# Performance work log

Hardware: AMD Instinct MI355X
Metric: run time of the kernel (lower is better)

## Reference

```python
import jax, jax.numpy as jnp
import numpy as np

N_NODES = 20000
N_EDGES = 320000
N_GRAPHS = 64
NEG_SLOPE = 0.2


def gat_conv(h, src, dst, a_src, a_dst, n_nodes):
    # h: [N, H, C] transformed node features; src/dst: [E] with self loops
    al_s = jnp.sum(h * a_src, axis=-1)  # [N, H]
    al_d = jnp.sum(h * a_dst, axis=-1)  # [N, H]
    e = jax.nn.leaky_relu(al_s[src] + al_d[dst], NEG_SLOPE)  # [E, H]
    m = jax.ops.segment_max(e, dst, num_segments=n_nodes)  # [N, H]
    ex = jnp.exp(e - m[dst])
    denom = jax.ops.segment_sum(ex, dst, num_segments=n_nodes)
    alpha = ex / denom[dst]  # [E, H] segment softmax over incoming edges
    # weighted scatter-aggregate of source features
    out = jax.ops.segment_sum(alpha[:, :, None] * h[src], dst, num_segments=n_nodes)
    return out  # [N, H, C]


def setup_inputs() -> dict:
    key = jax.random.key(0)
    ks = jax.random.split(key, 12)
    x = jax.random.normal(ks[0], (N_NODES, 3), dtype=jnp.float32)
    edge_index = jax.random.randint(ks[1], (2, N_EDGES), 0, N_NODES, dtype=jnp.int64)
    batch = jnp.sort(jax.random.randint(ks[2], (N_NODES,), 0, N_GRAPHS, dtype=jnp.int64))
    H1, C1 = 8, 8
    s = lambda fan_in: 1.0 / np.sqrt(fan_in)
    W1 = jax.random.normal(ks[3], (3, H1 * C1), dtype=jnp.float32) * s(3)
    a_src1 = jax.random.normal(ks[4], (H1, C1), dtype=jnp.float32) * s(C1)
    a_dst1 = jax.random.normal(ks[5], (H1, C1), dtype=jnp.float32) * s(C1)
    b1 = jnp.zeros((H1 * C1,), dtype=jnp.float32)
    W2 = jax.random.normal(ks[6], (H1 * C1, 512), dtype=jnp.float32) * s(H1 * C1)
    a_src2 = jax.random.normal(ks[7], (1, 512), dtype=jnp.float32) * s(512)
    a_dst2 = jax.random.normal(ks[8], (1, 512), dtype=jnp.float32) * s(512)
    b2 = jnp.zeros((512,), dtype=jnp.float32)
    Wo = jax.random.normal(ks[9], (512, 512), dtype=jnp.float32) * s(512)
    bo = jnp.zeros((512,), dtype=jnp.float32)
    return {"x": x, "edge_index": edge_index, "batch": batch,
            "W1": W1, "a_src1": a_src1, "a_dst1": a_dst1, "b1": b1,
            "W2": W2, "a_src2": a_src2, "a_dst2": a_dst2, "b2": b2,
            "Wo": Wo, "bo": bo}


def reference(x, edge_index, batch, W1, a_src1, a_dst1, b1,
              W2, a_src2, a_dst2, b2, Wo, bo):
    n = x.shape[0]
    loop = jnp.arange(n, dtype=edge_index.dtype)
    src = jnp.concatenate([edge_index[0], loop])
    dst = jnp.concatenate([edge_index[1], loop])
    # layer 1: 8 heads, concat
    h1 = (x @ W1).reshape(n, 8, 8)
    o1 = gat_conv(h1, src, dst, a_src1, a_dst1, n).reshape(n, 64) + b1
    o1 = jax.nn.elu(o1)
    # layer 2: 1 head, concat=False (mean over the single head)
    h2 = (o1 @ W2).reshape(n, 1, 512)
    o2 = gat_conv(h2, src, dst, a_src2, a_dst2, n)[:, 0, :] + b2
    o2 = jax.nn.elu(o2)
    # global mean pool per graph
    sums = jax.ops.segment_sum(o2, batch, num_segments=N_GRAPHS)
    cnt = jax.ops.segment_sum(jnp.ones((n,), dtype=o2.dtype), batch, num_segments=N_GRAPHS)
    pooled = sums / jnp.maximum(cnt, 1.0)[:, None]
    return pooled @ Wo + bo  # [G, 512]
```

## Files before the change

### kernel.cpp

```cpp
#include <hip/hip_runtime.h>
#include <math.h>

#define NN 20000
#define NE 320000
#define NT 340000
#define NG 64
#define HB 1329
#define CB 128
#define AB 2
#define SB 32

using short8  = __attribute__((ext_vector_type(8))) short;
using float4v = __attribute__((ext_vector_type(4))) float;

__device__ __forceinline__ float lrelu(float v) { return v > 0.f ? v : 0.2f * v; }
__device__ __forceinline__ float elu1(float v)  { return v > 0.f ? v : (expf(v) - 1.f); }
__device__ __forceinline__ float bflo(unsigned u) { return __uint_as_float(u << 16); }
__device__ __forceinline__ float bfhi(unsigned u) { return __uint_as_float(u & 0xFFFF0000u); }
__device__ __forceinline__ unsigned short f2bf(float f) {
    unsigned u = __float_as_uint(f);
    u += 0x7FFFu + ((u >> 16) & 1u);
    return (unsigned short)(u >> 16);
}

#define ACC8(ex, hv) \
    acc[0] = fmaf(ex, bflo(hv.x), acc[0]); \
    acc[1] = fmaf(ex, bfhi(hv.x), acc[1]); \
    acc[2] = fmaf(ex, bflo(hv.y), acc[2]); \
    acc[3] = fmaf(ex, bfhi(hv.y), acc[3]); \
    acc[4] = fmaf(ex, bflo(hv.z), acc[4]); \
    acc[5] = fmaf(ex, bfhi(hv.z), acc[5]); \
    acc[6] = fmaf(ex, bflo(hv.w), acc[6]); \
    acc[7] = fmaf(ex, bfhi(hv.w), acc[7]);

__global__ void k_prep(const int* __restrict__ ei, int* __restrict__ deg,
                       int* __restrict__ csr64,
                       const float* __restrict__ W2, unsigned short* __restrict__ W2bfT,
                       const float* __restrict__ as2, const float* __restrict__ ad2,
                       float* __restrict__ a2ps, float* __restrict__ a2pd,
                       const float* __restrict__ x, const float* __restrict__ W1,
                       const float* __restrict__ as1, const float* __restrict__ ad1,
                       unsigned short* __restrict__ h1bf, float* __restrict__ al_s,
                       float* __restrict__ al_d,
                       const int* __restrict__ batch, int* __restrict__ gstart,
                       float* __restrict__ sums) {
    int tid = threadIdx.x;
    int b = blockIdx.x;
    if (b < HB) {
        int t = b * 256 + tid;
        if (t < NT) {
            int s, d;
            if (t < NE) { s = ei[t]; d = ei[NE + t]; }
            else        { s = d = t - NE; }
            int r = atomicAdd(&deg[d], 1);
            if (r < 64) csr64[(d << 6) + r] = s;
        }
        return;
    }
    if (b < HB + CB) {
        int t = (b - HB) * 256 + tid;
        int k = t & 63, n = t >> 6;
        W2bfT[t] = f2bf(W2[k * 512 + n]);
        return;
    }
    if (b < HB + CB + AB) {
        __shared__ float pp[4][64];
        const float* av = (b == HB + CB) ? as2 : ad2;
        float* outp     = (b == HB + CB) ? a2ps : a2pd;
        int k = tid & 63, seg = tid >> 6;
        float s = 0.f;
        for (int j = seg * 128; j < seg * 128 + 128; ++j)
            s = fmaf(W2[k * 512 + j], av[j], s);
        pp[seg][k] = s;
        __syncthreads();
        if (tid < 64) outp[tid] = pp[0][tid] + pp[1][tid] + pp[2][tid] + pp[3][tid];
        return;
    }
    if (b < HB + CB + AB + SB) {
        int t = (b - HB - CB - AB) * 256 + tid;
        float4 zz = {0.f, 0.f, 0.f, 0.f};
        ((float4*)sums)[t] = zz;
        return;
    }
    if (b == HB + CB + AB + SB) {
        if (tid <= NG) {
            int lo = 0, hi = NN;
            while (lo < hi) {
                int mid = (lo + hi) >> 1;
                if (batch[mid] < tid) lo = mid + 1; else hi = mid;
            }
            gstart[tid] = lo;
        }
        return;
    }
    int n = (b - HB - CB - AB - SB - 1) * 4 + (tid >> 6);
    int j = tid & 63;
    float x0 = x[n * 3 + 0], x1 = x[n * 3 + 1], x2 = x[n * 3 + 2];
    float v = fmaf(x0, W1[j], fmaf(x1, W1[64 + j], x2 * W1[128 + j]));
    h1bf[n * 64 + j] = f2bf(v);
    float ps = v * as1[j];
    float pd = v * ad1[j];
    for (int o = 4; o >= 1; o >>= 1) {
        ps += __shfl_xor(ps, o, 8);
        pd += __shfl_xor(pd, o, 8);
    }
    if ((j & 7) == 0) {
        al_s[n * 8 + (j >> 3)] = ps;
        al_d[n * 8 + (j >> 3)] = pd;
    }
}

__global__ void k_l1(const int* __restrict__ deg, const int* __restrict__ csr64,
                     const float* __restrict__ al_s, const float* __restrict__ al_d,
                     const unsigned short* __restrict__ h1bf, const float* __restrict__ b1,
                     const float* __restrict__ a2ps, const float* __restrict__ a2pd,
                     unsigned short* __restrict__ o1bf, float* __restrict__ al_s2,
                     float* __restrict__ al_d2) {
    int nb = threadIdx.x >> 6;
    int n = blockIdx.x * 4 + nb;
    int lane = threadIdx.x & 63;
    int e8 = lane >> 3, c8 = lane & 7;
    int dg = deg[n]; dg = dg < 64 ? dg : 64;
    int sAll = csr64[(n << 6) + (lane < dg ? lane : 0)];
    float ald = al_d[n * 8 + c8];
    float acc[8] = {0.f, 0.f, 0.f, 0.f, 0.f, 0.f, 0.f, 0.f};
    float dsum = 0.f;
    for (int base = 0; base < dg; base += 16) {
        int sA = __shfl(sAll, base + e8, 64);
        int sB = __shfl(sAll, base + 8 + e8, 64);
        float exA = 0.f, exB = 0.f;
        if (base + e8 < dg)     exA = __expf(lrelu(al_s[sA * 8 + c8] + ald));
        if (base + 8 + e8 < dg) exB = __expf(lrelu(al_s[sB * 8 + c8] + ald));
        dsum += exA + exB;
        uint4 hA = *(const uint4*)(h1bf + sA * 64 + c8 * 8);
        uint4 hB = *(const uint4*)(h1bf + sB * 64 + c8 * 8);
        ACC8(exA, hA);
        ACC8(exB, hB);
    }
#pragma unroll
    for (int o = 32; o >= 8; o >>= 1) {
#pragma unroll
        for (int k = 0; k < 8; ++k) acc[k] += __shfl_xor(acc[k], o, 64);
        dsum += __shfl_xor(dsum, o, 64);
    }
    if (e8 == 0) {
        float inv = 1.f / dsum;
        const float* bp = b1 + c8 * 8;
        float v[8];
#pragma unroll
        for (int k = 0; k < 8; ++k) v[k] = elu1(acc[k] * inv + bp[k]);
        uint4 pk;
        pk.x = (unsigned)f2bf(v[0]) | ((unsigned)f2bf(v[1]) << 16);
        pk.y = (unsigned)f2bf(v[2]) | ((unsigned)f2bf(v[3]) << 16);
        pk.z = (unsigned)f2bf(v[4]) | ((unsigned)f2bf(v[5]) << 16);
        pk.w = (unsigned)f2bf(v[6]) | ((unsigned)f2bf(v[7]) << 16);
        *(uint4*)(o1bf + n * 64 + c8 * 8) = pk;
        float ps = 0.f, pd = 0.f;
        const float* asp = a2ps + c8 * 8;
        const float* adp = a2pd + c8 * 8;
#pragma unroll
        for (int k = 0; k < 8; ++k) {
            ps = fmaf(v[k], asp[k], ps);
            pd = fmaf(v[k], adp[k], pd);
        }
        for (int o = 4; o >= 1; o >>= 1) {
            ps += __shfl_xor(ps, o, 8);
            pd += __shfl_xor(pd, o, 8);
        }
        if (c8 == 0) { al_s2[n] = ps; al_d2[n] = pd; }
    }
}

__global__ void k_l2gemm(const int* __restrict__ deg, const int* __restrict__ csr64,
                         const float* __restrict__ al_s2, const float* __restrict__ al_d2,
                         const unsigned short* __restrict__ o1bf,
                         const unsigned short* __restrict__ W2bfT,
                         const float* __restrict__ b2, const int* __restrict__ batch,
                         float* __restrict__ sums) {
    __shared__ unsigned short lagg[16][72];
    int n0 = blockIdx.x * 16;
    int w = threadIdx.x >> 6, lane = threadIdx.x & 63;
    int e8 = lane >> 3, c8 = lane & 7;
#pragma unroll
    for (int i = 0; i < 2; ++i) {
        int r = w * 2 + i;
        int n = n0 + r;
        float ald = al_d2[n];
        int dg = deg[n]; dg = dg < 64 ? dg : 64;
        int sAll = csr64[(n << 6) + (lane < dg ? lane : 0)];
        float exAll = 0.f;
        if (lane < dg) exAll = __expf(lrelu(al_s2[sAll] + ald));
        float dsum = exAll;
        dsum += __shfl_xor(dsum, 1, 64);
        dsum += __shfl_xor(dsum, 2, 64);
        dsum += __shfl_xor(dsum, 4, 64);
        float acc[8] = {0.f, 0.f, 0.f, 0.f, 0.f, 0.f, 0.f, 0.f};
        for (int base = 0; base < dg; base += 16) {
            int sA   = __shfl(sAll, base + e8, 64);
            int sB   = __shfl(sAll, base + 8 + e8, 64);
            float exA = __shfl(exAll, base + e8, 64);
            float exB = __shfl(exAll, base + 8 + e8, 64);
            uint4 hA = *(const uint4*)(o1bf + sA * 64 + c8 * 8);
            uint4 hB = *(const uint4*)(o1bf + sB * 64 + c8 * 8);
            ACC8(exA, hA);
            ACC8(exB, hB);
        }
#pragma unroll
        for (int o = 32; o >= 8; o >>= 1) {
#pragma unroll
            for (int k = 0; k < 8; ++k) acc[k] += __shfl_xor(acc[k], o, 64);
            dsum += __shfl_xor(dsum, o, 64);
        }
        if (e8 == 0) {
            float inv = 1.f / dsum;
            uint4 pk;
            pk.x = (unsigned)f2bf(acc[0] * inv) | ((unsigned)f2bf(acc[1] * inv) << 16);
            pk.y = (unsigned)f2bf(acc[2] * inv) | ((unsigned)f2bf(acc[3] * inv) << 16);
            pk.z = (unsigned)f2bf(acc[4] * inv) | ((unsigned)f2bf(acc[5] * inv) << 16);
            pk.w = (unsigned)f2bf(acc[6] * inv) | ((unsigned)f2bf(acc[7] * inv) << 16);
            *(uint4*)&lagg[r][c8 * 8] = pk;
        }
    }
    __syncthreads();
    int mcol = lane & 15;
    int q = lane >> 4;
    short8 a0 = *(const short8*)&lagg[mcol][q * 8];
    short8 a1 = *(const short8*)&lagg[mcol][32 + q * 8];
    int gmin = batch[n0], gmax = batch[n0 + 15];
    int batchq[4];
#pragma unroll
    for (int r = 0; r < 4; ++r) batchq[r] = batch[n0 + q * 4 + r];
#pragma unroll
    for (int t = 0; t < 4; ++t) {
        int c = w * 64 + t * 16 + mcol;
        const unsigned short* bp = W2bfT + c * 64 + q * 8;
        short8 b0 = *(const short8*)bp;
        short8 b1v = *(const short8*)(bp + 32);
        float4v acc = {0.f, 0.f, 0.f, 0.f};
        acc = __builtin_amdgcn_mfma_f32_16x16x32_bf16(a0, b0, acc, 0, 0, 0);
        acc = __builtin_amdgcn_mfma_f32_16x16x32_bf16(a1, b1v, acc, 0, 0, 0);
        float bias = b2[c];
        float val[4];
#pragma unroll
        for (int r = 0; r < 4; ++r) val[r] = elu1(acc[r] + bias);
        for (int g = gmin; g <= gmax; ++g) {
            float s = 0.f;
#pragma unroll
            for (int r = 0; r < 4; ++r) s += (batchq[r] == g) ? val[r] : 0.f;
            s += __shfl_xor(s, 16, 64);
            s += __shfl_xor(s, 32, 64);
            if (q == 0) atomicAdd(&sums[g * 512 + c], s);
        }
    }
}

__global__ void k_final(const float* __restrict__ sums, const int* __restrict__ gstart,
                        const float* __restrict__ Wo, const float* __restrict__ bo,
                        float* __restrict__ out) {
    __shared__ float sp[512];
    int g = blockIdx.x >> 3;
    int j = (blockIdx.x & 7) * 64 + threadIdx.x;
    for (int k = threadIdx.x; k < 512; k += 64) sp[k] = sums[g * 512 + k];
    __syncthreads();
    float c = (float)(gstart[g + 1] - gstart[g]);
    float inv = 1.f / (c > 0.f ? c : 1.f);
    float acc = 0.f;
    for (int k = 0; k < 512; ++k) acc = fmaf(sp[k], Wo[k * 512 + j], acc);
    out[g * 512 + j] = fmaf(acc, inv, bo[j]);
}

extern "C" void kernel_launch(void* const* d_in, const int* in_sizes, int n_in,
                              void* d_out, int out_size, void* d_ws, size_t ws_size,
                              hipStream_t stream) {
    const float* x     = (const float*)d_in[0];
    const int*   ei    = (const int*)d_in[1];
    const int*   batch = (const int*)d_in[2];
    const float* W1    = (const float*)d_in[3];
    const float* as1   = (const float*)d_in[4];
    const float* ad1   = (const float*)d_in[5];
    const float* b1    = (const float*)d_in[6];
    const float* W2    = (const float*)d_in[7];
    const float* as2   = (const float*)d_in[8];
    const float* ad2   = (const float*)d_in[9];
    const float* b2    = (const float*)d_in[10];
    const float* Wo    = (const float*)d_in[11];
    const float* bo    = (const float*)d_in[12];
    float* out = (float*)d_out;

    float* w = (float*)d_ws;
    unsigned short* h1bf  = (unsigned short*)(w + 0);
    float* al_s1 = w + 640000;
    float* al_d1 = w + 800000;
    unsigned short* o1bf  = (unsigned short*)(w + 960000);
    unsigned short* W2bfT = (unsigned short*)(w + 1600000);
    float* a2ps  = w + 1616384;
    float* a2pd  = w + 1616448;
    float* al_s2 = w + 1616512;
    float* al_d2 = w + 1636512;
    int*   gstart = (int*)(w + 1656512);
    int*   csr64  = (int*)(w + 1656580);
    float* sums   = w + 2936580;
    int*   deg    = (int*)(w + 2969348);

    hipMemsetAsync(deg, 0, (size_t)20000 * 4, stream);

    k_prep   <<<HB + CB + AB + SB + 1 + NN / 4, 256, 0, stream>>>(
        ei, deg, csr64, W2, W2bfT, as2, ad2, a2ps, a2pd,
        x, W1, as1, ad1, h1bf, al_s1, al_d1, batch, gstart, sums);
    k_l1     <<<NN / 4, 256, 0, stream>>>(deg, csr64, al_s1, al_d1, h1bf, b1,
                                          a2ps, a2pd, o1bf, al_s2, al_d2);
    k_l2gemm <<<NN / 16, 512, 0, stream>>>(deg, csr64, al_s2, al_d2, o1bf,
                                           W2bfT, b2, batch, sums);
    k_final  <<<NG * 8, 64, 0, stream>>>(sums, gstart, Wo, bo, out);
}
```

Measured before the change: 162.4 us.

## Fuse all stages into one persistent cooperative kernel with grid syncs

Replaces the memset plus four kernel launches with a single cooperative kernel of 512 blocks that runs every stage in grid-stride loops, separated by grid-wide barriers. The aim is to remove launch overhead and inter-kernel gaps. The layer-2 GEMM tile now uses 256-thread blocks, each wave covering 128 output columns. The final projection splits K across four waves and reduces the partials in shared memory. In exchange it adds the cost of four grid barriers and limits occupancy to the fixed persistent grid, which may hurt the latency-bound gather phases.

```diff
diff --git a/kernel.cpp b/kernel.cpp
--- a/kernel.cpp
+++ b/kernel.cpp
@@ -1,14 +1,17 @@
 #include <hip/hip_runtime.h>
+#include <hip/hip_cooperative_groups.h>
 #include <math.h>
+
+namespace cg = cooperative_groups;
 
 #define NN 20000
 #define NE 320000
 #define NT 340000
 #define NG 64
-#define HB 1329
-#define CB 128
-#define AB 2
-#define SB 32
+#define GRID 512
+#define TPB 256
+#define NTH (GRID * TPB)
+#define NWV (GRID * 4)
 
 using short8  = __attribute__((ext_vector_type(8))) short;
 using float4v = __attribute__((ext_vector_type(4))) float;
@@ -33,175 +36,97 @@
     acc[6] = fmaf(ex, bflo(hv.w), acc[6]); \
     acc[7] = fmaf(ex, bfhi(hv.w), acc[7]);
 
-__global__ void k_prep(const int* __restrict__ ei, int* __restrict__ deg,
-                       int* __restrict__ csr64,
-                       const float* __restrict__ W2, unsigned short* __restrict__ W2bfT,
-                       const float* __restrict__ as2, const float* __restrict__ ad2,
-                       float* __restrict__ a2ps, float* __restrict__ a2pd,
-                       const float* __restrict__ x, const float* __restrict__ W1,
-                       const float* __restrict__ as1, const float* __restrict__ ad1,
-                       unsigned short* __restrict__ h1bf, float* __restrict__ al_s,
-                       float* __restrict__ al_d,
-                       const int* __restrict__ batch, int* __restrict__ gstart,
-                       float* __restrict__ sums) {
-    int tid = threadIdx.x;
-    int b = blockIdx.x;
-    if (b < HB) {
-        int t = b * 256 + tid;
-        if (t < NT) {
-            int s, d;
-            if (t < NE) { s = ei[t]; d = ei[NE + t]; }
-            else        { s = d = t - NE; }
-            int r = atomicAdd(&deg[d], 1);
-            if (r < 64) csr64[(d << 6) + r] = s;
-        }
-        return;
-    }
-    if (b < HB + CB) {
-        int t = (b - HB) * 256 + tid;
+__global__ __launch_bounds__(TPB, 2) void k_all(
+    const int* __restrict__ ei, const float* __restrict__ x,
+    const int* __restrict__ batch, const float* __restrict__ W1,
+    const float* __restrict__ as1, const float* __restrict__ ad1,
+    const float* __restrict__ b1, const float* __restrict__ W2,
+    const float* __restrict__ as2, const float* __restrict__ ad2,
+    const float* __restrict__ b2, const float* __restrict__ Wo,
+    const float* __restrict__ bo,
+    int* __restrict__ deg, int* __restrict__ csr64,
+    unsigned short* __restrict__ W2bfT,
+    float* __restrict__ a2ps, float* __restrict__ a2pd,
+    unsigned short* __restrict__ h1bf,
+    float* __restrict__ al_s1, float* __restrict__ al_d1,
+    unsigned short* __restrict__ o1bf,
+    float* __restrict__ al_s2, float* __restrict__ al_d2,
+    int* __restrict__ gstart, float* __restrict__ sums,
+    float* __restrict__ out)
+{
+    cg::grid_group gg = cg::this_grid();
+    __shared__ __align__(16) char smraw[2304];
+
+    int tid  = threadIdx.x, bid = blockIdx.x;
+    int gtid = bid * TPB + tid;
+    int lane = tid & 63, wv = tid >> 6;
+    int gw   = bid * 4 + wv;
+    int e8   = lane >> 3, c8 = lane & 7;
+
+    for (int i = gtid; i < NN; i += NTH) deg[i] = 0;
+    for (int i = gtid; i < NG * 512; i += NTH) sums[i] = 0.f;
+    for (int t = gtid; t < 64 * 512; t += NTH) {
         int k = t & 63, n = t >> 6;
         W2bfT[t] = f2bf(W2[k * 512 + n]);
-        return;
-    }
-    if (b < HB + CB + AB) {
-        __shared__ float pp[4][64];
-        const float* av = (b == HB + CB) ? as2 : ad2;
-        float* outp     = (b == HB + CB) ? a2ps : a2pd;
-        int k = tid & 63, seg = tid >> 6;
+    }
+    if (gw < 128) {
+        int which = gw >> 6, k = gw & 63;
+        const float* av = which ? ad2 : as2;
         float s = 0.f;
-        for (int j = seg * 128; j < seg * 128 + 128; ++j)
-            s = fmaf(W2[k * 512 + j], av[j], s);
-        pp[seg][k] = s;
-        __syncthreads();
-        if (tid < 64) outp[tid] = pp[0][tid] + pp[1][tid] + pp[2][tid] + pp[3][tid];
-        return;
-    }
-    if (b < HB + CB + AB + SB) {
-        int t = (b - HB - CB - AB) * 256 + tid;
-        float4 zz = {0.f, 0.f, 0.f, 0.f};
-        ((float4*)sums)[t] = zz;
-        return;
-    }
-    if (b == HB + CB + AB + SB) {
-        if (tid <= NG) {
-            int lo = 0, hi = NN;
-            while (lo < hi) {
-                int mid = (lo + hi) >> 1;
-                if (batch[mid] < tid) lo = mid + 1; else hi = mid;
-            }
-            gstart[tid] = lo;
-        }
-        return;
-    }
-    int n = (b - HB - CB - AB - SB - 1) * 4 + (tid >> 6);
-    int j = tid & 63;
-    float x0 = x[n * 3 + 0], x1 = x[n * 3 + 1], x2 = x[n * 3 + 2];
-    float v = fmaf(x0, W1[j], fmaf(x1, W1[64 + j], x2 * W1[128 + j]));
-    h1bf[n * 64 + j] = f2bf(v);
-    float ps = v * as1[j];
-    float pd = v * ad1[j];
-    for (int o = 4; o >= 1; o >>= 1) {
-        ps += __shfl_xor(ps, o, 8);
-        pd += __shfl_xor(pd, o, 8);
-    }
-    if ((j & 7) == 0) {
-        al_s[n * 8 + (j >> 3)] = ps;
-        al_d[n * 8 + (j >> 3)] = pd;
-    }
-}
-
-__global__ void k_l1(const int* __restrict__ deg, const int* __restrict__ csr64,
-                     const float* __restrict__ al_s, const float* __restrict__ al_d,
-                     const unsigned short* __restrict__ h1bf, const float* __restrict__ b1,
-                     const float* __restrict__ a2ps, const float* __restrict__ a2pd,
-                     unsigned short* __restrict__ o1bf, float* __restrict__ al_s2,
-                     float* __restrict__ al_d2) {
-    int nb = threadIdx.x >> 6;
-    int n = blockIdx.x * 4 + nb;
-    int lane = threadIdx.x & 63;
-    int e8 = lane >> 3, c8 = lane & 7;
-    int dg = deg[n]; dg = dg < 64 ? dg : 64;
-    int sAll = csr64[(n << 6) + (lane < dg ? lane : 0)];
-    float ald = al_d[n * 8 + c8];
-    float acc[8] = {0.f, 0.f, 0.f, 0.f, 0.f, 0.f, 0.f, 0.f};
-    float dsum = 0.f;
-    for (int base = 0; base < dg; base += 16) {
-        int sA = __shfl(sAll, base + e8, 64);
-        int sB = __shfl(sAll, base + 8 + e8, 64);
-        float exA = 0.f, exB = 0.f;
-        if (base + e8 < dg)     exA = __expf(lrelu(al_s[sA * 8 + c8] + ald));
-        if (base + 8 + e8 < dg) exB = __expf(lrelu(al_s[sB * 8 + c8] + ald));
-        dsum += exA + exB;
-        uint4 hA = *(const uint4*)(h1bf + sA * 64 + c8 * 8);
-        uint4 hB = *(const uint4*)(h1bf + sB * 64 + c8 * 8);
-        ACC8(exA, hA);
-        ACC8(exB, hB);
-    }
-#pragma unroll
-    for (int o = 32; o >= 8; o >>= 1) {
-#pragma unroll
-        for (int k = 0; k < 8; ++k) acc[k] += __shfl_xor(acc[k], o, 64);
-        dsum += __shfl_xor(dsum, o, 64);
-    }
-    if (e8 == 0) {
-        float inv = 1.f / dsum;
-        const float* bp = b1 + c8 * 8;
-        float v[8];
-#pragma unroll
-        for (int k = 0; k < 8; ++k) v[k] = elu1(acc[k] * inv + bp[k]);
-        uint4 pk;
-        pk.x = (unsigned)f2bf(v[0]) | ((unsigned)f2bf(v[1]) << 16);
-        pk.y = (unsigned)f2bf(v[2]) | ((unsigned)f2bf(v[3]) << 16);
-        pk.z = (unsigned)f2bf(v[4]) | ((unsigned)f2bf(v[5]) << 16);
-        pk.w = (unsigned)f2bf(v[6]) | ((unsigned)f2bf(v[7]) << 16);
-        *(uint4*)(o1bf + n * 64 + c8 * 8) = pk;
-        float ps = 0.f, pd = 0.f;
-        const float* asp = a2ps + c8 * 8;
-        const float* adp = a2pd + c8 * 8;
-#pragma unroll
-        for (int k = 0; k < 8; ++k) {
-            ps = fmaf(v[k], asp[k], ps);
-            pd = fmaf(v[k], adp[k], pd);
-        }
+        for (int j = lane; j < 512; j += 64) s = fmaf(W2[k * 512 + j], av[j], s);
+#pragma unroll
+        for (int o = 32; o >= 1; o >>= 1) s += __shfl_xor(s, o, 64);
+        if (lane == 0) (which ? a2pd : a2ps)[k] = s;
+    }
+    if (gtid <= NG) {
+        int lo = 0, hi = NN;
+        while (lo < hi) {
+            int mid = (lo + hi) >> 1;
+            if (batch[mid] < gtid) lo = mid + 1; else hi = mid;
+        }
+        gstart[gtid] = lo;
+    }
+    for (int t = gtid; t < NN * 64; t += NTH) {
+        int n = t >> 6, j = t & 63;
+        float x0 = x[n * 3 + 0], x1 = x[n * 3 + 1], x2 = x[n * 3 + 2];
+        float v = fmaf(x0, W1[j], fmaf(x1, W1[64 + j], x2 * W1[128 + j]));
+        h1bf[n * 64 + j] = f2bf(v);
+        float ps = v * as1[j], pd = v * ad1[j];
         for (int o = 4; o >= 1; o >>= 1) {
             ps += __shfl_xor(ps, o, 8);
             pd += __shfl_xor(pd, o, 8);
         }
-        if (c8 == 0) { al_s2[n] = ps; al_d2[n] = pd; }
-    }
-}
-
-__global__ void k_l2gemm(const int* __restrict__ deg, const int* __restrict__ csr64,
-                         const float* __restrict__ al_s2, const float* __restrict__ al_d2,
-                         const unsigned short* __restrict__ o1bf,
-                         const unsigned short* __restrict__ W2bfT,
-                         const float* __restrict__ b2, const int* __restrict__ batch,
-                         float* __restrict__ sums) {
-    __shared__ unsigned short lagg[16][72];
-    int n0 = blockIdx.x * 16;
-    int w = threadIdx.x >> 6, lane = threadIdx.x & 63;
-    int e8 = lane >> 3, c8 = lane & 7;
-#pragma unroll
-    for (int i = 0; i < 2; ++i) {
-        int r = w * 2 + i;
-        int n = n0 + r;
-        float ald = al_d2[n];
+        if ((j & 7) == 0) {
+            al_s1[n * 8 + (j >> 3)] = ps;
+            al_d1[n * 8 + (j >> 3)] = pd;
+        }
+    }
+    gg.sync();
+
+    for (int t = gtid; t < NT; t += NTH) {
+        int s, d;
+        if (t < NE) { s = ei[t]; d = ei[NE + t]; }
+        else        { s = d = t - NE; }
+        int r = atomicAdd(&deg[d], 1);
+        if (r < 64) csr64[(d << 6) + r] = s;
+    }
+    gg.sync();
+
+    for (int n = gw; n < NN; n += NWV) {
         int dg = deg[n]; dg = dg < 64 ? dg : 64;
         int sAll = csr64[(n << 6) + (lane < dg ? lane : 0)];
-        float exAll = 0.f;
-        if (lane < dg) exAll = __expf(lrelu(al_s2[sAll] + ald));
-        float dsum = exAll;
-        dsum += __shfl_xor(dsum, 1, 64);
-        dsum += __shfl_xor(dsum, 2, 64);
-        dsum += __shfl_xor(dsum, 4, 64);
+        float ald = al_d1[n * 8 + c8];
         float acc[8] = {0.f, 0.f, 0.f, 0.f, 0.f, 0.f, 0.f, 0.f};
+        float dsum = 0.f;
         for (int base = 0; base < dg; base += 16) {
-            int sA   = __shfl(sAll, base + e8, 64);
-            int sB   = __shfl(sAll, base + 8 + e8, 64);
-            float exA = __shfl(exAll, base + e8, 64);
-            float exB = __shfl(exAll, base + 8 + e8, 64);
-            uint4 hA = *(const uint4*)(o1bf + sA * 64 + c8 * 8);
-            uint4 hB = *(const uint4*)(o1bf + sB * 64 + c8 * 8);
+            int sA = __shfl(sAll, base + e8, 64);
+            int sB = __shfl(sAll, base + 8 + e8, 64);
+            float exA = 0.f, exB = 0.f;
+            if (base + e8 < dg)     exA = __expf(lrelu(al_s1[sA * 8 + c8] + ald));
+            if (base + 8 + e8 < dg) exB = __expf(lrelu(al_s1[sB * 8 + c8] + ald));
+            dsum += exA + exB;
+            uint4 hA = *(const uint4*)(h1bf + sA * 64 + c8 * 8);
+            uint4 hB = *(const uint4*)(h1bf + sB * 64 + c8 * 8);
             ACC8(exA, hA);
             ACC8(exB, hB);
         }
@@ -213,60 +138,130 @@
         }
         if (e8 == 0) {
             float inv = 1.f / dsum;
+            const float* bp = b1 + c8 * 8;
+            float v[8];
+#pragma unroll
+            for (int k = 0; k < 8; ++k) v[k] = elu1(acc[k] * inv + bp[k]);
             uint4 pk;
-            pk.x = (unsigned)f2bf(acc[0] * inv) | ((unsigned)f2bf(acc[1] * inv) << 16);
-            pk.y = (unsigned)f2bf(acc[2] * inv) | ((unsigned)f2bf(acc[3] * inv) << 16);
-            pk.z = (unsigned)f2bf(acc[4] * inv) | ((unsigned)f2bf(acc[5] * inv) << 16);
-            pk.w = (unsigned)f2bf(acc[6] * inv) | ((unsigned)f2bf(acc[7] * inv) << 16);
-            *(uint4*)&lagg[r][c8 * 8] = pk;
-        }
-    }
-    __syncthreads();
-    int mcol = lane & 15;
-    int q = lane >> 4;
-    short8 a0 = *(const short8*)&lagg[mcol][q * 8];
-    short8 a1 = *(const short8*)&lagg[mcol][32 + q * 8];
-    int gmin = batch[n0], gmax = batch[n0 + 15];
-    int batchq[4];
-#pragma unroll
-    for (int r = 0; r < 4; ++r) batchq[r] = batch[n0 + q * 4 + r];
-#pragma unroll
-    for (int t = 0; t < 4; ++t) {
-        int c = w * 64 + t * 16 + mcol;
-        const unsigned short* bp = W2bfT + c * 64 + q * 8;
-        short8 b0 = *(const short8*)bp;
-        short8 b1v = *(const short8*)(bp + 32);
-        float4v acc = {0.f, 0.f, 0.f, 0.f};
-        acc = __builtin_amdgcn_mfma_f32_16x16x32_bf16(a0, b0, acc, 0, 0, 0);
-        acc = __builtin_amdgcn_mfma_f32_16x16x32_bf16(a1, b1v, acc, 0, 0, 0);
-        float bias = b2[c];
-        float val[4];
-#pragma unroll
-        for (int r = 0; r < 4; ++r) val[r] = elu1(acc[r] + bias);
-        for (int g = gmin; g <= gmax; ++g) {
-            float s = 0.f;
-#pragma unroll
-            for (int r = 0; r < 4; ++r) s += (batchq[r] == g) ? val[r] : 0.f;
-            s += __shfl_xor(s, 16, 64);
-            s += __shfl_xor(s, 32, 64);
-            if (q == 0) atomicAdd(&sums[g * 512 + c], s);
-        }
-    }
-}
-
-__global__ void k_final(const float* __restrict__ sums, const int* __restrict__ gstart,
-                        const float* __restrict__ Wo, const float* __restrict__ bo,
-                        float* __restrict__ out) {
-    __shared__ float sp[512];
-    int g = blockIdx.x >> 3;
-    int j = (blockIdx.x & 7) * 64 + threadIdx.x;
-    for (int k = threadIdx.x; k < 512; k += 64) sp[k] = sums[g * 512 + k];
-    __syncthreads();
-    float c = (float)(gstart[g + 1] - gstart[g]);
-    float inv = 1.f / (c > 0.f ? c : 1.f);
-    float acc = 0.f;
-    for (int k = 0; k < 512; ++k) acc = fmaf(sp[k], Wo[k * 512 + j], acc);
-    out[g * 512 + j] = fmaf(acc, inv, bo[j]);
+            pk.x = (unsigned)f2bf(v[0]) | ((unsigned)f2bf(v[1]) << 16);
+            pk.y = (unsigned)f2bf(v[2]) | ((unsigned)f2bf(v[3]) << 16);
+            pk.z = (unsigned)f2bf(v[4]) | ((unsigned)f2bf(v[5]) << 16);
+            pk.w = (unsigned)f2bf(v[6]) | ((unsigned)f2bf(v[7]) << 16);
+            *(uint4*)(o1bf + n * 64 + c8 * 8) = pk;
+            float ps = 0.f, pd = 0.f;
+            const float* asp = a2ps + c8 * 8;
+            const float* adp = a2pd + c8 * 8;
+#pragma unroll
+            for (int k = 0; k < 8; ++k) {
+                ps = fmaf(v[k], asp[k], ps);
+                pd = fmaf(v[k], adp[k], pd);
+            }
+            for (int o = 4; o >= 1; o >>= 1) {
+                ps += __shfl_xor(ps, o, 8);
+                pd += __shfl_xor(pd, o, 8);
+            }
+            if (c8 == 0) { al_s2[n] = ps; al_d2[n] = pd; }
+        }
+    }
+    gg.sync();
+
+    {
+        unsigned short (*lagg)[72] = (unsigned short(*)[72])smraw;
+        for (int tile = bid; tile < NN / 16; tile += GRID) {
+            int n0 = tile * 16;
+#pragma unroll
+            for (int i = 0; i < 4; ++i) {
+                int r = wv * 4 + i;
+                int n = n0 + r;
+                float ald = al_d2[n];
+                int dg = deg[n]; dg = dg < 64 ? dg : 64;
+                int sAll = csr64[(n << 6) + (lane < dg ? lane : 0)];
+                float exAll = 0.f;
+                if (lane < dg) exAll = __expf(lrelu(al_s2[sAll] + ald));
+                float dsum = exAll;
+                dsum += __shfl_xor(dsum, 1, 64);
+                dsum += __shfl_xor(dsum, 2, 64);
+                dsum += __shfl_xor(dsum, 4, 64);
+                float acc[8] = {0.f, 0.f, 0.f, 0.f, 0.f, 0.f, 0.f, 0.f};
+                for (int base = 0; base < dg; base += 16) {
+                    int sA    = __shfl(sAll, base + e8, 64);
+                    int sB    = __shfl(sAll, base + 8 + e8, 64);
+                    float exA = __shfl(exAll, base + e8, 64);
+                    float exB = __shfl(exAll, base + 8 + e8, 64);
+                    uint4 hA = *(const uint4*)(o1bf + sA * 64 + c8 * 8);
+                    uint4 hB = *(const uint4*)(o1bf + sB * 64 + c8 * 8);
+                    ACC8(exA, hA);
+                    ACC8(exB, hB);
+                }
+#pragma unroll
+                for (int o = 32; o >= 8; o >>= 1) {
+#pragma unroll
+                    for (int k = 0; k < 8; ++k) acc[k] += __shfl_xor(acc[k], o, 64);
+                    dsum += __shfl_xor(dsum, o, 64);
+                }
+                if (e8 == 0) {
+                    float inv = 1.f / dsum;
+                    uint4 pk;
+                    pk.x = (unsigned)f2bf(acc[0] * inv) | ((unsigned)f2bf(acc[1] * inv) << 16);
+                    pk.y = (unsigned)f2bf(acc[2] * inv) | ((unsigned)f2bf(acc[3] * inv) << 16);
+                    pk.z = (unsigned)f2bf(acc[4] * inv) | ((unsigned)f2bf(acc[5] * inv) << 16);
+                    pk.w = (unsigned)f2bf(acc[6] * inv) | ((unsigned)f2bf(acc[7] * inv) << 16);
+                    *(uint4*)&lagg[r][c8 * 8] = pk;
+                }
+            }
+            __syncthreads();
+            int mcol = lane & 15;
+            int q = lane >> 4;
+            short8 a0 = *(const short8*)&lagg[mcol][q * 8];
+            short8 a1 = *(const short8*)&lagg[mcol][32 + q * 8];
+            __syncthreads();
+            int gmin = batch[n0], gmax = batch[n0 + 15];
+            int batchq[4];
+#pragma unroll
+            for (int r = 0; r < 4; ++r) batchq[r] = batch[n0 + q * 4 + r];
+#pragma unroll
+            for (int t = 0; t < 8; ++t) {
+                int c = wv * 128 + t * 16 + mcol;
+                const unsigned short* bp = W2bfT + c * 64 + q * 8;
+                short8 b0  = *(const short8*)bp;
+                short8 b1v = *(const short8*)(bp + 32);
+                float4v macc = {0.f, 0.f, 0.f, 0.f};
+                macc = __builtin_amdgcn_mfma_f32_16x16x32_bf16(a0, b0, macc, 0, 0, 0);
+                macc = __builtin_amdgcn_mfma_f32_16x16x32_bf16(a1, b1v, macc, 0, 0, 0);
+                float bias = b2[c];
+                float val[4];
+#pragma unroll
+                for (int r = 0; r < 4; ++r) val[r] = elu1(macc[r] + bias);
+                for (int g = gmin; g <= gmax; ++g) {
+                    float s = 0.f;
+#pragma unroll
+                    for (int r = 0; r < 4; ++r) s += (batchq[r] == g) ? val[r] : 0.f;
+                    s += __shfl_xor(s, 16, 64);
+                    s += __shfl_xor(s, 32, 64);
+                    if (q == 0) atomicAdd(&sums[g * 512 + c], s);
+                }
+            }
+        }
+    }
+    gg.sync();
+
+    {
+        float (*part)[64] = (float(*)[64])smraw;
+        int g = bid >> 3, jo = bid & 7;
+        int j = jo * 64 + lane;
+        const float* srow = sums + g * 512;
+        float acc = 0.f;
+        for (int k = wv * 128; k < wv * 128 + 128; ++k)
+            acc = fmaf(srow[k], Wo[k * 512 + j], acc);
+        part[wv][lane] = acc;
+        __syncthreads();
+        if (tid < 64) {
+            float s = part[0][tid] + part[1][tid] + part[2][tid] + part[3][tid];
+            float c = (float)(gstart[g + 1] - gstart[g]);
+            float inv = 1.f / (c > 0.f ? c : 1.f);
+            out[g * 512 + jo * 64 + tid] = fmaf(s, inv, bo[jo * 64 + tid]);
+        }
+    }
 }
 
 extern "C" void kernel_launch(void* const* d_in, const int* in_sizes, int n_in,
@@ -302,14 +297,12 @@
     float* sums   = w + 2936580;
     int*   deg    = (int*)(w + 2969348);
 
-    hipMemsetAsync(deg, 0, (size_t)20000 * 4, stream);
-
-    k_prep   <<<HB + CB + AB + SB + 1 + NN / 4, 256, 0, stream>>>(
-        ei, deg, csr64, W2, W2bfT, as2, ad2, a2ps, a2pd,
-        x, W1, as1, ad1, h1bf, al_s1, al_d1, batch, gstart, sums);
-    k_l1     <<<NN / 4, 256, 0, stream>>>(deg, csr64, al_s1, al_d1, h1bf, b1,
-                                          a2ps, a2pd, o1bf, al_s2, al_d2);
-    k_l2gemm <<<NN / 16, 512, 0, stream>>>(deg, csr64, al_s2, al_d2, o1bf,
-                                           W2bfT, b2, batch, sums);
-    k_final  <<<NG * 8, 64, 0, stream>>>(sums, gstart, Wo, bo, out);
+    void* args[] = {
+        (void*)&ei, (void*)&x, (void*)&batch, (void*)&W1, (void*)&as1, (void*)&ad1,
+        (void*)&b1, (void*)&W2, (void*)&as2, (void*)&ad2, (void*)&b2, (void*)&Wo,
+        (void*)&bo, (void*)&deg, (void*)&csr64, (void*)&W2bfT, (void*)&a2ps,
+        (void*)&a2pd, (void*)&h1bf, (void*)&al_s1, (void*)&al_d1, (void*)&o1bf,
+        (void*)&al_s2, (void*)&al_d2, (void*)&gstart, (void*)&sums, (void*)&out
+    };
+    hipLaunchCooperativeKernel((const void*)k_all, dim3(GRID), dim3(TPB), args, 0, stream);
 }
```

After: 420.5 us. 159% more time.

## Fuse final pooled GEMM into l2gemm via last-blocks completion counter

Applied to the files above, without the earlier changes.

The separate final kernel is removed. Its pooled-feature times Wo work now runs inside the layer-2 kernel: the last 256 blocks to finish, counted with an atomic, spin-wait until all blocks are done and then compute one graph and one 128-column slice each, splitting K four ways through shared memory. Zeroing of the sums buffer moves from the prep kernel into a single memset that also clears deg and the counter. This saves a kernel launch and its tail, at the cost of spin-waiting blocks that rely on the last arrivals being resident together.

```diff
diff --git a/kernel.cpp b/kernel.cpp
--- a/kernel.cpp
+++ b/kernel.cpp
@@ -8,7 +8,8 @@
 #define HB 1329
 #define CB 128
 #define AB 2
-#define SB 32
+#define NB2 (NN / 16)
+#define NFIN 256
 
 using short8  = __attribute__((ext_vector_type(8))) short;
 using float4v = __attribute__((ext_vector_type(4))) float;
@@ -42,8 +43,7 @@
                        const float* __restrict__ as1, const float* __restrict__ ad1,
                        unsigned short* __restrict__ h1bf, float* __restrict__ al_s,
                        float* __restrict__ al_d,
-                       const int* __restrict__ batch, int* __restrict__ gstart,
-                       float* __restrict__ sums) {
+                       const int* __restrict__ batch, int* __restrict__ gstart) {
     int tid = threadIdx.x;
     int b = blockIdx.x;
     if (b < HB) {
@@ -76,13 +76,7 @@
         if (tid < 64) outp[tid] = pp[0][tid] + pp[1][tid] + pp[2][tid] + pp[3][tid];
         return;
     }
-    if (b < HB + CB + AB + SB) {
-        int t = (b - HB - CB - AB) * 256 + tid;
-        float4 zz = {0.f, 0.f, 0.f, 0.f};
-        ((float4*)sums)[t] = zz;
-        return;
-    }
-    if (b == HB + CB + AB + SB) {
+    if (b == HB + CB + AB) {
         if (tid <= NG) {
             int lo = 0, hi = NN;
             while (lo < hi) {
@@ -93,7 +87,7 @@
         }
         return;
     }
-    int n = (b - HB - CB - AB - SB - 1) * 4 + (tid >> 6);
+    int n = (b - HB - CB - AB - 1) * 4 + (tid >> 6);
     int j = tid & 63;
     float x0 = x[n * 3 + 0], x1 = x[n * 3 + 1], x2 = x[n * 3 + 2];
     float v = fmaf(x0, W1[j], fmaf(x1, W1[64 + j], x2 * W1[128 + j]));
@@ -176,14 +170,19 @@
                          const unsigned short* __restrict__ o1bf,
                          const unsigned short* __restrict__ W2bfT,
                          const float* __restrict__ b2, const int* __restrict__ batch,
-                         float* __restrict__ sums) {
-    __shared__ unsigned short lagg[16][72];
+                         float* __restrict__ sums,
+                         const float* __restrict__ Wo, const float* __restrict__ bo,
+                         const int* __restrict__ gstart, int* __restrict__ done,
+                         float* __restrict__ out) {
+    __shared__ __align__(16) char smraw[4096];
+    __shared__ int s_old;
+    unsigned short (*lagg)[72] = (unsigned short(*)[72])smraw;
     int n0 = blockIdx.x * 16;
-    int w = threadIdx.x >> 6, lane = threadIdx.x & 63;
+    int wv = threadIdx.x >> 6, lane = threadIdx.x & 63;
     int e8 = lane >> 3, c8 = lane & 7;
 #pragma unroll
     for (int i = 0; i < 2; ++i) {
-        int r = w * 2 + i;
+        int r = wv * 2 + i;
         int n = n0 + r;
         float ald = al_d2[n];
         int dg = deg[n]; dg = dg < 64 ? dg : 64;
@@ -232,17 +231,17 @@
     for (int r = 0; r < 4; ++r) batchq[r] = batch[n0 + q * 4 + r];
 #pragma unroll
     for (int t = 0; t < 4; ++t) {
-        int c = w * 64 + t * 16 + mcol;
+        int c = wv * 64 + t * 16 + mcol;
         const unsigned short* bp = W2bfT + c * 64 + q * 8;
         short8 b0 = *(const short8*)bp;
         short8 b1v = *(const short8*)(bp + 32);
-        float4v acc = {0.f, 0.f, 0.f, 0.f};
-        acc = __builtin_amdgcn_mfma_f32_16x16x32_bf16(a0, b0, acc, 0, 0, 0);
-        acc = __builtin_amdgcn_mfma_f32_16x16x32_bf16(a1, b1v, acc, 0, 0, 0);
+        float4v macc = {0.f, 0.f, 0.f, 0.f};
+        macc = __builtin_amdgcn_mfma_f32_16x16x32_bf16(a0, b0, macc, 0, 0, 0);
+        macc = __builtin_amdgcn_mfma_f32_16x16x32_bf16(a1, b1v, macc, 0, 0, 0);
         float bias = b2[c];
         float val[4];
 #pragma unroll
-        for (int r = 0; r < 4; ++r) val[r] = elu1(acc[r] + bias);
+        for (int r = 0; r < 4; ++r) val[r] = elu1(macc[r] + bias);
         for (int g = gmin; g <= gmax; ++g) {
             float s = 0.f;
 #pragma unroll
@@ -252,21 +251,43 @@
             if (q == 0) atomicAdd(&sums[g * 512 + c], s);
         }
     }
-}
-
-__global__ void k_final(const float* __restrict__ sums, const int* __restrict__ gstart,
-                        const float* __restrict__ Wo, const float* __restrict__ bo,
-                        float* __restrict__ out) {
-    __shared__ float sp[512];
-    int g = blockIdx.x >> 3;
-    int j = (blockIdx.x & 7) * 64 + threadIdx.x;
-    for (int k = threadIdx.x; k < 512; k += 64) sp[k] = sums[g * 512 + k];
-    __syncthreads();
-    float c = (float)(gstart[g + 1] - gstart[g]);
-    float inv = 1.f / (c > 0.f ? c : 1.f);
+
+    __syncthreads();
+    if (threadIdx.x == 0) {
+        __threadfence();
+        s_old = atomicAdd(done, 1);
+    }
+    __syncthreads();
+    int claim = s_old - (NB2 - NFIN);
+    if (claim < 0) return;
+    if (threadIdx.x == 0) {
+        while (__hip_atomic_load(done, __ATOMIC_ACQUIRE, __HIP_MEMORY_SCOPE_AGENT) < NB2)
+            __builtin_amdgcn_s_sleep(2);
+    }
+    __syncthreads();
+    __threadfence();
+    float* sp = (float*)smraw;
+    float (*part)[128] = (float(*)[128])(smraw + 2048);
+    int g = claim >> 2, jo = claim & 3;
+    const float* srow = sums + g * 512;
+    for (int k = threadIdx.x; k < 512; k += 512)
+        sp[k] = __hip_atomic_load(&srow[k], __ATOMIC_RELAXED, __HIP_MEMORY_SCOPE_AGENT);
+    __syncthreads();
+    int jj = threadIdx.x & 127;
+    int kq = threadIdx.x >> 7;
+    int j  = jo * 128 + jj;
     float acc = 0.f;
-    for (int k = 0; k < 512; ++k) acc = fmaf(sp[k], Wo[k * 512 + j], acc);
-    out[g * 512 + j] = fmaf(acc, inv, bo[j]);
+    for (int k = kq * 128; k < kq * 128 + 128; ++k)
+        acc = fmaf(sp[k], Wo[k * 512 + j], acc);
+    part[kq][jj] = acc;
+    __syncthreads();
+    if (threadIdx.x < 128) {
+        float s = part[0][threadIdx.x] + part[1][threadIdx.x]
+                + part[2][threadIdx.x] + part[3][threadIdx.x];
+        float c = (float)(gstart[g + 1] - gstart[g]);
+        float inv = 1.f / (c > 0.f ? c : 1.f);
+        out[g * 512 + jo * 128 + threadIdx.x] = fmaf(s, inv, bo[jo * 128 + threadIdx.x]);
+    }
 }
 
 extern "C" void kernel_launch(void* const* d_in, const int* in_sizes, int n_in,
@@ -301,15 +322,16 @@
     int*   csr64  = (int*)(w + 1656580);
     float* sums   = w + 2936580;
     int*   deg    = (int*)(w + 2969348);
-
-    hipMemsetAsync(deg, 0, (size_t)20000 * 4, stream);
-
-    k_prep   <<<HB + CB + AB + SB + 1 + NN / 4, 256, 0, stream>>>(
+    int*   done   = (int*)(w + 2989348);
+
+    hipMemsetAsync(sums, 0, (size_t)(32768 + 20000 + 4) * 4, stream);
+
+    k_prep   <<<HB + CB + AB + 1 + NN / 4, 256, 0, stream>>>(
         ei, deg, csr64, W2, W2bfT, as2, ad2, a2ps, a2pd,
-        x, W1, as1, ad1, h1bf, al_s1, al_d1, batch, gstart, sums);
+        x, W1, as1, ad1, h1bf, al_s1, al_d1, batch, gstart);
     k_l1     <<<NN / 4, 256, 0, stream>>>(deg, csr64, al_s1, al_d1, h1bf, b1,
                                           a2ps, a2pd, o1bf, al_s2, al_d2);
-    k_l2gemm <<<NN / 16, 512, 0, stream>>>(deg, csr64, al_s2, al_d2, o1bf,
-                                           W2bfT, b2, batch, sums);
-    k_final  <<<NG * 8, 64, 0, stream>>>(sums, gstart, Wo, bo, out);
-}
+    k_l2gemm <<<NB2, 512, 0, stream>>>(deg, csr64, al_s2, al_d2, o1bf,
+                                       W2bfT, b2, batch, sums,
+                                       Wo, bo, gstart, done, out);
+}
```

Result: slower. 259.2 us (+59.7%).
